# Kernel optimization log

Hardware: AMD Instinct MI355X
Metric: run time of the kernel (lower is better)

Reference implementation:

```python
import jax, jax.numpy as jnp
import numpy as np

T, B, H = 256, 64, 1024

def setup_inputs() -> dict:
    key = jax.random.key(0)
    k0, k1, k2, k3 = jax.random.split(key, 4)
    x = jax.random.normal(k0, (T, B, H), dtype=jnp.float32)
    # episode resets are sparse events
    resets = jax.random.bernoulli(k1, 0.01, (T, B))
    h0 = jnp.zeros((B, H), dtype=jnp.float32)  # flax GRUCell.initialize_carry -> zeros
    s = np.float32(1.0 / np.sqrt(H))
    Wi = jax.random.normal(k2, (H, 3 * H), dtype=jnp.float32) * s  # packed [ir|iz|in]
    Wh = jax.random.normal(k3, (H, 3 * H), dtype=jnp.float32) * s  # packed [hr|hz|hn]
    bi = jnp.zeros((3 * H,), dtype=jnp.float32)
    bn = jnp.zeros((H,), dtype=jnp.float32)  # only the 'n' hidden dense has a bias in flax
    return dict(x=x, resets=resets, h0=h0, Wi=Wi, bi=bi, Wh=Wh, bn=bn)

def reference(x, resets, h0, Wi, bi, Wh, bn):
    """Scanned GRU with reset masking, matching flax nn.scan(GRUCell)."""
    def step(h, inp):
        x_t, r_t = inp  # [B,H], [B]
        h = jnp.where(r_t[:, None], jnp.zeros_like(h), h)  # reset carry to initial (zeros)
        gi = x_t @ Wi + bi          # [B,3H]
        gh = h @ Wh                 # [B,3H]
        ir, iz, inn = jnp.split(gi, 3, axis=-1)
        hr, hz, hn = jnp.split(gh, 3, axis=-1)
        r = jax.nn.sigmoid(ir + hr)
        z = jax.nn.sigmoid(iz + hz)
        n = jnp.tanh(inn + r * (hn + bn))
        h_new = (1.0 - z) * n + z * h
        return h_new, h_new  # GRUCell returns (new_state, y=new_state)
    h_final, ys = jax.lax.scan(step, h0, (x, resets))
    return h_final, ys
```

## Files before the change

### kernel.cpp

```cpp
#include <hip/hip_runtime.h>
#include <hip/hip_bf16.h>
#include <cstdint>


#define TT 256
#define BB 64
#define HH 1024
#define H3 3072

typedef __attribute__((ext_vector_type(8))) short s16x8;
typedef __attribute__((ext_vector_type(4))) float f32x4;
typedef __attribute__((ext_vector_type(4))) unsigned int u32x4;
typedef unsigned long long ull;

__device__ __forceinline__ float fast_sigmoid(float x) {
  float e = __expf(-fabsf(x));
  float s = 1.0f / (1.0f + e);
  return x >= 0.0f ? s : 1.0f - s;
}
__device__ __forceinline__ float fast_tanh(float x) {
  float e = __expf(-2.0f * fabsf(x));
  float t = (1.0f - e) / (1.0f + e);
  return x >= 0.0f ? t : -t;
}
__device__ __forceinline__ f32x4 mfma16(s16x8 a, s16x8 b, f32x4 c) {
  return __builtin_amdgcn_mfma_f32_16x16x32_bf16(a, b, c, 0, 0, 0);
}

#define LD8(p) __hip_atomic_load((p), __ATOMIC_RELAXED, __HIP_MEMORY_SCOPE_AGENT)


__global__ void k_cvt_x(const float* __restrict__ x, __hip_bfloat16* __restrict__ xb, int n) {
  int i = (blockIdx.x * blockDim.x + threadIdx.x) * 4;
  if (i + 3 < n) {
    float4 v = *reinterpret_cast<const float4*>(x + i);
    xb[i + 0] = __float2bfloat16(v.x);
    xb[i + 1] = __float2bfloat16(v.y);
    xb[i + 2] = __float2bfloat16(v.z);
    xb[i + 3] = __float2bfloat16(v.w);
  }
}

__global__ void k_transpose_w(const float* __restrict__ W, __hip_bfloat16* __restrict__ WT) {
  __shared__ float tile[32][33];
  int c0 = blockIdx.x * 32, r0 = blockIdx.y * 32;
  int tx = threadIdx.x & 31, ty = threadIdx.x >> 5;
#pragma unroll
  for (int i = 0; i < 32; i += 8)
    tile[ty + i][tx] = W[(size_t)(r0 + ty + i) * H3 + c0 + tx];
  __syncthreads();
#pragma unroll
  for (int i = 0; i < 32; i += 8)
    WT[(size_t)(c0 + ty + i) * HH + r0 + tx] = __float2bfloat16(tile[tx][ty + i]);
}


template <bool GIF32>
__global__ __launch_bounds__(256, 2) void k_gemm_gi(
    const __hip_bfloat16* __restrict__ A,
    const __hip_bfloat16* __restrict__ Bt,
    const float* __restrict__ bi,
    void* __restrict__ gi)
{
  __shared__ __align__(16) __hip_bfloat16 As[128 * 32];
  __shared__ __align__(16) __hip_bfloat16 Bs[128 * 32];
  const int bid = blockIdx.x;
  const int mt = bid / 24, nt = bid % 24;
  const int m0 = mt * 128, n0 = nt * 128;
  const int tid = threadIdx.x, lane = tid & 63, w = tid >> 6;
  const int wm = w & 1, wn = w >> 1;

  f32x4 acc[4][4];
#pragma unroll
  for (int ai = 0; ai < 4; ++ai)
#pragma unroll
    for (int bj = 0; bj < 4; ++bj) acc[ai][bj] = (f32x4){0.f, 0.f, 0.f, 0.f};

  for (int k0 = 0; k0 < HH; k0 += 32) {
#pragma unroll
    for (int i = 0; i < 2; ++i) {
      const int c = w + i * 4;
      const int idx = c * 64 + lane;
      const int row = idx >> 2, slot = idx & 3;
      __builtin_amdgcn_global_load_lds(
          (const __attribute__((address_space(1))) void*)(A + (size_t)(m0 + row) * HH + k0 + slot * 8),
          (__attribute__((address_space(3))) void*)(As + c * 512), 16, 0, 0);
      __builtin_amdgcn_global_load_lds(
          (const __attribute__((address_space(1))) void*)(Bt + (size_t)(n0 + row) * HH + k0 + slot * 8),
          (__attribute__((address_space(3))) void*)(Bs + c * 512), 16, 0, 0);
    }
    __syncthreads();
    s16x8 af[4], bf[4];
#pragma unroll
    for (int ai = 0; ai < 4; ++ai) {
      int r = wm * 64 + ai * 16 + (lane & 15);
      af[ai] = *reinterpret_cast<const s16x8*>(As + r * 32 + (lane >> 4) * 8);
    }
#pragma unroll
    for (int bj = 0; bj < 4; ++bj) {
      int r = wn * 64 + bj * 16 + (lane & 15);
      bf[bj] = *reinterpret_cast<const s16x8*>(Bs + r * 32 + (lane >> 4) * 8);
    }
#pragma unroll
    for (int ai = 0; ai < 4; ++ai)
#pragma unroll
      for (int bj = 0; bj < 4; ++bj) acc[ai][bj] = mfma16(af[ai], bf[bj], acc[ai][bj]);
    __syncthreads();
  }

#pragma unroll
  for (int ai = 0; ai < 4; ++ai) {
#pragma unroll
    for (int reg = 0; reg < 4; ++reg) {
      const size_t row = (size_t)m0 + wm * 64 + ai * 16 + (lane >> 4) * 4 + reg;
#pragma unroll
      for (int bj = 0; bj < 4; ++bj) {
        const int col = n0 + wn * 64 + bj * 16 + (lane & 15);
        float v = acc[ai][bj][reg] + bi[col];
        if (GIF32)
          reinterpret_cast<float*>(gi)[row * H3 + col] = v;
        else
          reinterpret_cast<__hip_bfloat16*>(gi)[row * H3 + col] = __float2bfloat16(v);
      }
    }
  }
}


template <bool GIF32>
__global__ __launch_bounds__(256, 1) void k_gru(
    const void* __restrict__ gi_,
    const int* __restrict__ resets,
    const float* __restrict__ h0,
    const float* __restrict__ bn,
    const __hip_bfloat16* __restrict__ WhT,
    __hip_bfloat16* hseq,
    float* __restrict__ out)
{
  __shared__ __align__(16) __hip_bfloat16 Bsh[48 * 1024];
  __shared__ __align__(16) f32x4 part[2][4][3][64];
  __shared__ __align__(8) __hip_bfloat16 hsh[16][16];
  const int tid = threadIdx.x;
  const int wave = tid >> 6, lane = tid & 63;
  const int wg = blockIdx.x;
  const int g = (wg & 7) >> 1;
  const int s = ((wg >> 3) << 1) | (wg & 1);
  const int bg0 = g * 16, j0 = s * 16;

  for (int cch = tid; cch < 48 * 128; cch += 256) {
    const int row = cch >> 7, slot = cch & 127;
    const int gate = row >> 4, jj = row & 15;
    u32x4 v = *reinterpret_cast<const u32x4*>(WhT + (size_t)(gate * HH + j0 + jj) * HH + slot * 8);
    const int byte = row * 2048 + ((slot * 16) ^ ((row & 7) << 4));
    *reinterpret_cast<u32x4*>(reinterpret_cast<char*>(Bsh) + byte) = v;
  }

  const int jl = lane & 15;
  const int bh = (lane >> 4) * 4;
  const int prow = lane >> 2, pq = (lane & 3) * 4;
  const int al = lane & 15;
  const int koff = (lane >> 4) * 8;
  const int j = j0 + jl;

  const char* bbase = reinterpret_cast<const char*>(Bsh);
  const int xsw = (jl & 7) << 4;
  const int rb0 = jl * 2048, rb1 = (16 + jl) * 2048, rb2 = (32 + jl) * 2048;

  float hp[4];
  float girC[4], gizC[4], ginC[4];
  int rstEC[4];
  float bnj = 0.f;

  if (wave == 0) {
    bnj = bn[j];
#pragma unroll
    for (int r = 0; r < 4; ++r) hp[r] = h0[(size_t)(bg0 + bh + r) * HH + j0 + jl];
#pragma unroll
    for (int r = 0; r < 4; ++r) hsh[bh + r][jl] = __float2bfloat16(hp[r]);
    ull pv = *reinterpret_cast<const ull*>(&hsh[prow][pq]);
    __hip_atomic_store(reinterpret_cast<ull*>(hseq + (size_t)g * 16384 + prow * HH + j0 + pq),
                       pv, __ATOMIC_RELAXED, __HIP_MEMORY_SCOPE_AGENT);
#pragma unroll
    for (int r = 0; r < 4; ++r) {
      const int b = bg0 + bh + r;
      rstEC[r] = resets[b];
      if (GIF32) {
        const float* grow = reinterpret_cast<const float*>(gi_) + (size_t)b * H3;
        girC[r] = grow[j]; gizC[r] = grow[HH + j]; ginC[r] = grow[2 * HH + j];
      } else {
        const __hip_bfloat16* grow = reinterpret_cast<const __hip_bfloat16*>(gi_) + (size_t)b * H3;
        girC[r] = __bfloat162float(grow[j]);
        gizC[r] = __bfloat162float(grow[HH + j]);
        ginC[r] = __bfloat162float(grow[2 * HH + j]);
      }
    }
  }
  __syncthreads();

  for (int t = 0; t < TT; ++t) {
    const int rstA = resets[t * BB + bg0 + al];
    const __hip_bfloat16* rd = hseq + (size_t)t * 65536 + g * 16384;
    const ull* ch = reinterpret_cast<const ull*>(rd + al * HH + koff) + wave * 64;

    {
      int gq = 0;
      ull can;
      do {
        can = LD8(ch + 57);
      } while (__any((int)(can == ~0ull)) && ++gq < (1 << 22));
    }
    ull w[16];
#pragma unroll
    for (int i = 0; i < 8; ++i) {
      w[2 * i + 0] = LD8(ch + i * 8 + 0);
      w[2 * i + 1] = LD8(ch + i * 8 + 1);
    }
    {
      int gq = 0;
      for (;;) {
        unsigned bad = 0;
#pragma unroll
        for (int i = 0; i < 16; ++i) bad |= (unsigned)(w[i] == ~0ull);
        if (!__any((int)bad) || ++gq >= (1 << 20)) break;
#pragma unroll
        for (int i = 0; i < 8; ++i) {
          w[2 * i + 0] = LD8(ch + i * 8 + 0);
          w[2 * i + 1] = LD8(ch + i * 8 + 1);
        }
      }
    }

    const ull amask = rstA ? 0ull : ~0ull;
    f32x4 aR = {0.f, 0.f, 0.f, 0.f}, aZ = {0.f, 0.f, 0.f, 0.f}, aN = {0.f, 0.f, 0.f, 0.f};
#pragma unroll
    for (int i = 0; i < 8; ++i) {
      const int kk = wave * 8 + i;
      union { ull q[2]; s16x8 v; } u;
      u.q[0] = w[2 * i + 0] & amask;
      u.q[1] = w[2 * i + 1] & amask;
      const int kb = kk * 64 + (lane >> 4) * 16;
      s16x8 b0 = *reinterpret_cast<const s16x8*>(bbase + rb0 + (kb ^ xsw));
      s16x8 b1 = *reinterpret_cast<const s16x8*>(bbase + rb1 + (kb ^ xsw));
      s16x8 b2 = *reinterpret_cast<const s16x8*>(bbase + rb2 + (kb ^ xsw));
      aR = mfma16(u.v, b0, aR);
      aZ = mfma16(u.v, b1, aZ);
      aN = mfma16(u.v, b2, aN);
    }

    const int p = t & 1;
    part[p][wave][0][lane] = aR;
    part[p][wave][1][lane] = aZ;
    part[p][wave][2][lane] = aN;
    __syncthreads();

    if (wave == 0) {
      f32x4 sR = part[p][0][0][lane], sZ = part[p][0][1][lane], sN = part[p][0][2][lane];
#pragma unroll
      for (int ww = 1; ww < 4; ++ww) {
        sR += part[p][ww][0][lane];
        sZ += part[p][ww][1][lane];
        sN += part[p][ww][2][lane];
      }
      float hnew[4];
#pragma unroll
      for (int r = 0; r < 4; ++r) {
        const float hprev = rstEC[r] ? 0.f : hp[r];
        const float rg = fast_sigmoid(girC[r] + sR[r]);
        const float zg = fast_sigmoid(gizC[r] + sZ[r]);
        const float ng = fast_tanh(ginC[r] + rg * (sN[r] + bnj));
        hnew[r] = (1.0f - zg) * ng + zg * hprev;
        hp[r] = hnew[r];
      }
#pragma unroll
      for (int r = 0; r < 4; ++r) hsh[bh + r][jl] = __float2bfloat16(hnew[r]);
      ull pv = *reinterpret_cast<const ull*>(&hsh[prow][pq]);
      __hip_atomic_store(
          reinterpret_cast<ull*>(hseq + (size_t)(t + 1) * 65536 + g * 16384 + prow * HH + j0 + pq),
          pv, __ATOMIC_RELAXED, __HIP_MEMORY_SCOPE_AGENT);

      float* ys = out + 65536 + (size_t)t * 65536;
#pragma unroll
      for (int r = 0; r < 4; ++r)
        __builtin_nontemporal_store(hnew[r], &ys[(size_t)(bg0 + bh + r) * HH + j]);

      const int tn = (t + 1 < TT) ? t + 1 : t;
#pragma unroll
      for (int r = 0; r < 4; ++r) {
        const int b = bg0 + bh + r;
        rstEC[r] = resets[tn * BB + b];
        if (GIF32) {
          const float* grow = reinterpret_cast<const float*>(gi_) + (size_t)(tn * BB + b) * H3;
          girC[r] = grow[j]; gizC[r] = grow[HH + j]; ginC[r] = grow[2 * HH + j];
        } else {
          const __hip_bfloat16* grow =
              reinterpret_cast<const __hip_bfloat16*>(gi_) + (size_t)(tn * BB + b) * H3;
          girC[r] = __bfloat162float(grow[j]);
          gizC[r] = __bfloat162float(grow[HH + j]);
          ginC[r] = __bfloat162float(grow[2 * HH + j]);
        }
      }
    }
  }

  if (wave == 0) {
#pragma unroll
    for (int r = 0; r < 4; ++r)
      out[(size_t)(bg0 + bh + r) * HH + j0 + jl] = hp[r];
  }
}


extern "C" void kernel_launch(void* const* d_in, const int* in_sizes, int n_in,
                              void* d_out, int out_size, void* d_ws, size_t ws_size,
                              hipStream_t stream) {
  const float* x      = (const float*)d_in[0];
  const int* resets   = (const int*)d_in[1];
  const float* h0     = (const float*)d_in[2];
  const float* Wi     = (const float*)d_in[3];
  const float* bi     = (const float*)d_in[4];
  const float* Wh     = (const float*)d_in[5];
  const float* bn     = (const float*)d_in[6];
  (void)in_sizes; (void)n_in; (void)out_size;

  char* ws = (char*)d_ws;
  __hip_bfloat16* xb   = (__hip_bfloat16*)(ws);
  __hip_bfloat16* hseq = (__hip_bfloat16*)(ws);
  __hip_bfloat16* WiT  = (__hip_bfloat16*)(ws + 33685504);
  __hip_bfloat16* WhT  = (__hip_bfloat16*)(ws + 39976960);
  void* gi             = (void*)(ws + 46268416);

  const bool gif32 = ws_size >= 46268416ull + (size_t)16384 * 3072 * 4;

  k_cvt_x<<<16384, 256, 0, stream>>>(x, xb, TT * BB * HH);
  k_transpose_w<<<dim3(96, 32), 256, 0, stream>>>(Wi, WiT);
  k_transpose_w<<<dim3(96, 32), 256, 0, stream>>>(Wh, WhT);
  if (gif32) {
    k_gemm_gi<true><<<3072, 256, 0, stream>>>(xb, WiT, bi, gi);
    hipMemsetAsync(hseq, 0xFF, 33685504, stream);
    k_gru<true><<<256, 256, 0, stream>>>(gi, resets, h0, bn, WhT, hseq, (float*)d_out);
  } else {
    k_gemm_gi<false><<<3072, 256, 0, stream>>>(xb, WiT, bi, gi);
    hipMemsetAsync(hseq, 0xFF, 33685504, stream);
    k_gru<false><<<256, 256, 0, stream>>>(gi, resets, h0, bn, WhT, hseq, (float*)d_out);
  }
}
```

Baseline: 1.413 ms.

## Keep Wh slice in registers, retile GRU blocks, use cache-bypassing sentinel polling

The persistent GRU kernel now gives each block 8 batch rows and 32 hidden columns instead of 16x16. Each wave holds its share of the recurrent weight slice in registers, so the LDS weight buffer and its per-step shared-memory reads go away. Cross-block hidden-state exchange now uses inline-asm loads with cache-scope bits (sc0, escalating to sc0 sc1) and stores written twice, once with sc0 sc1, to make polling and publishing cheaper. A custom sentinel-fill kernel replaces hipMemsetAsync. In exchange, register pressure rises sharply with 48 s16x8 fragments per lane, half the MFMA rows are masked padding, and the code depends on precise hardware cache semantics.

```diff
diff --git a/kernel.cpp b/kernel.cpp
--- a/kernel.cpp
+++ b/kernel.cpp
@@ -27,7 +27,60 @@
   return __builtin_amdgcn_mfma_f32_16x16x32_bf16(a, b, c, 0, 0, 0);
 }
 
-#define LD8(p) __hip_atomic_load((p), __ATOMIC_RELAXED, __HIP_MEMORY_SCOPE_AGENT)
+
+__device__ __forceinline__ u32x4 ld16c(const char* p, bool e) {
+  u32x4 r;
+  if (!e)
+    asm volatile("global_load_dwordx4 %0, %1, off sc0\n\t"
+                 "s_waitcnt vmcnt(0)"
+                 : "=&v"(r) : "v"(p) : "memory");
+  else
+    asm volatile("global_load_dwordx4 %0, %1, off sc0 sc1\n\t"
+                 "s_waitcnt vmcnt(0)"
+                 : "=&v"(r) : "v"(p) : "memory");
+  return r;
+}
+
+__device__ __forceinline__ void ld8_sc0(u32x4 (&W)[8], const char* b) {
+  asm volatile(
+      "global_load_dwordx4 %0, %8, off sc0\n\t"
+      "global_load_dwordx4 %1, %8, off offset:64 sc0\n\t"
+      "global_load_dwordx4 %2, %8, off offset:128 sc0\n\t"
+      "global_load_dwordx4 %3, %8, off offset:192 sc0\n\t"
+      "global_load_dwordx4 %4, %8, off offset:256 sc0\n\t"
+      "global_load_dwordx4 %5, %8, off offset:320 sc0\n\t"
+      "global_load_dwordx4 %6, %8, off offset:384 sc0\n\t"
+      "global_load_dwordx4 %7, %8, off offset:448 sc0\n\t"
+      "s_waitcnt vmcnt(0)"
+      : "=&v"(W[0]), "=&v"(W[1]), "=&v"(W[2]), "=&v"(W[3]),
+        "=&v"(W[4]), "=&v"(W[5]), "=&v"(W[6]), "=&v"(W[7])
+      : "v"(b) : "memory");
+}
+__device__ __forceinline__ void ld8_sc1(u32x4 (&W)[8], const char* b) {
+  asm volatile(
+      "global_load_dwordx4 %0, %8, off sc0 sc1\n\t"
+      "global_load_dwordx4 %1, %8, off offset:64 sc0 sc1\n\t"
+      "global_load_dwordx4 %2, %8, off offset:128 sc0 sc1\n\t"
+      "global_load_dwordx4 %3, %8, off offset:192 sc0 sc1\n\t"
+      "global_load_dwordx4 %4, %8, off offset:256 sc0 sc1\n\t"
+      "global_load_dwordx4 %5, %8, off offset:320 sc0 sc1\n\t"
+      "global_load_dwordx4 %6, %8, off offset:384 sc0 sc1\n\t"
+      "global_load_dwordx4 %7, %8, off offset:448 sc0 sc1\n\t"
+      "s_waitcnt vmcnt(0)"
+      : "=&v"(W[0]), "=&v"(W[1]), "=&v"(W[2]), "=&v"(W[3]),
+        "=&v"(W[4]), "=&v"(W[5]), "=&v"(W[6]), "=&v"(W[7])
+      : "v"(b) : "memory");
+}
+
+__device__ __forceinline__ void st8_pub(char* p, ull v) {
+  asm volatile("global_store_dwordx2 %0, %1, off\n\t"
+               "global_store_dwordx2 %0, %1, off sc0 sc1"
+               :: "v"(p), "v"(v) : "memory");
+}
+
+__device__ __forceinline__ unsigned sentq(const u32x4& v) {
+  return (unsigned)(((v[0] & v[1]) == ~0u) | ((v[2] & v[3]) == ~0u));
+}
 
 
 __global__ void k_cvt_x(const float* __restrict__ x, __hip_bfloat16* __restrict__ xb, int n) {
@@ -52,6 +105,12 @@
 #pragma unroll
   for (int i = 0; i < 32; i += 8)
     WT[(size_t)(c0 + ty + i) * HH + r0 + tx] = __float2bfloat16(tile[tx][ty + i]);
+}
+
+__global__ void k_fill_sentinel(ull* __restrict__ p, int nwords) {
+  int idx = blockIdx.x * blockDim.x + threadIdx.x;
+  for (int i = idx; i < nwords; i += gridDim.x * blockDim.x)
+    __hip_atomic_store(p + i, ~0ull, __ATOMIC_RELAXED, __HIP_MEMORY_SCOPE_AGENT);
 }
 
 
@@ -137,175 +196,162 @@
     __hip_bfloat16* hseq,
     float* __restrict__ out)
 {
-  __shared__ __align__(16) __hip_bfloat16 Bsh[48 * 1024];
-  __shared__ __align__(16) f32x4 part[2][4][3][64];
-  __shared__ __align__(8) __hip_bfloat16 hsh[16][16];
+  __shared__ __align__(16) f32x4 part[2][4][6][32];
+  __shared__ __align__(8) __hip_bfloat16 hshW[4][8][8];
+
   const int tid = threadIdx.x;
   const int wave = tid >> 6, lane = tid & 63;
   const int wg = blockIdx.x;
-  const int g = (wg & 7) >> 1;
-  const int s = ((wg >> 3) << 1) | (wg & 1);
-  const int bg0 = g * 16, j0 = s * 16;
-
-  for (int cch = tid; cch < 48 * 128; cch += 256) {
-    const int row = cch >> 7, slot = cch & 127;
-    const int gate = row >> 4, jj = row & 15;
-    u32x4 v = *reinterpret_cast<const u32x4*>(WhT + (size_t)(gate * HH + j0 + jj) * HH + slot * 8);
-    const int byte = row * 2048 + ((slot * 16) ^ ((row & 7) << 4));
-    *reinterpret_cast<u32x4*>(reinterpret_cast<char*>(Bsh) + byte) = v;
-  }
-
-  const int jl = lane & 15;
-  const int bh = (lane >> 4) * 4;
-  const int prow = lane >> 2, pq = (lane & 3) * 4;
-  const int al = lane & 15;
-  const int koff = (lane >> 4) * 8;
-  const int j = j0 + jl;
-
-  const char* bbase = reinterpret_cast<const char*>(Bsh);
-  const int xsw = (jl & 7) << 4;
-  const int rb0 = jl * 2048, rb1 = (16 + jl) * 2048, rb2 = (32 + jl) * 2048;
-
-  float hp[4];
-  float girC[4], gizC[4], ginC[4];
-  int rstEC[4];
+  const int g = wg & 7;
+  const int s = wg >> 3;
+  const int bg0 = g * 8, j0 = s * 32;
+  const int lq = lane >> 4, lc = lane & 15;
+
+  s16x8 bf[6][8];
+#pragma unroll
+  for (int gate = 0; gate < 3; ++gate)
+#pragma unroll
+    for (int nt = 0; nt < 2; ++nt)
+#pragma unroll
+      for (int kk = 0; kk < 8; ++kk)
+        bf[gate * 2 + nt][kk] = *reinterpret_cast<const s16x8*>(
+            WhT + (size_t)(gate * HH + j0 + nt * 16 + lc) * HH + wave * 256 + kk * 32 + lq * 8);
+
+  const int colg = j0 + 8 * wave + (lane & 7);
+  const int brow0 = bg0 + ((lane >> 3) & 1) * 4;
+  float hp[4], giR[4], giZ[4], giN[4];
+  int rstE[4];
   float bnj = 0.f;
-
-  if (wave == 0) {
-    bnj = bn[j];
-#pragma unroll
-    for (int r = 0; r < 4; ++r) hp[r] = h0[(size_t)(bg0 + bh + r) * HH + j0 + jl];
-#pragma unroll
-    for (int r = 0; r < 4; ++r) hsh[bh + r][jl] = __float2bfloat16(hp[r]);
-    ull pv = *reinterpret_cast<const ull*>(&hsh[prow][pq]);
-    __hip_atomic_store(reinterpret_cast<ull*>(hseq + (size_t)g * 16384 + prow * HH + j0 + pq),
-                       pv, __ATOMIC_RELAXED, __HIP_MEMORY_SCOPE_AGENT);
-#pragma unroll
-    for (int r = 0; r < 4; ++r) {
-      const int b = bg0 + bh + r;
-      rstEC[r] = resets[b];
+  char* const hseqB = reinterpret_cast<char*>(hseq);
+
+  if (lane < 16) {
+    bnj = bn[colg];
+#pragma unroll
+    for (int i = 0; i < 4; ++i) {
+      const int b = brow0 + i;
+      hp[i] = h0[(size_t)b * HH + colg];
+      rstE[i] = resets[b];
       if (GIF32) {
         const float* grow = reinterpret_cast<const float*>(gi_) + (size_t)b * H3;
-        girC[r] = grow[j]; gizC[r] = grow[HH + j]; ginC[r] = grow[2 * HH + j];
+        giR[i] = grow[colg]; giZ[i] = grow[HH + colg]; giN[i] = grow[2 * HH + colg];
       } else {
-        const __hip_bfloat16* grow = reinterpret_cast<const __hip_bfloat16*>(gi_) + (size_t)b * H3;
-        girC[r] = __bfloat162float(grow[j]);
-        gizC[r] = __bfloat162float(grow[HH + j]);
-        ginC[r] = __bfloat162float(grow[2 * HH + j]);
-      }
-    }
-  }
-  __syncthreads();
+        const __hip_bfloat16* grow =
+            reinterpret_cast<const __hip_bfloat16*>(gi_) + (size_t)b * H3;
+        giR[i] = __bfloat162float(grow[colg]);
+        giZ[i] = __bfloat162float(grow[HH + colg]);
+        giN[i] = __bfloat162float(grow[2 * HH + colg]);
+      }
+      hshW[wave][(b - bg0)][lane & 7] = __float2bfloat16(hp[i]);
+    }
+    ull pv = *reinterpret_cast<const ull*>(&hshW[wave][lane >> 1][(lane & 1) * 4]);
+    st8_pub(hseqB + ((size_t)(bg0 + (lane >> 1)) * HH + j0 + 8 * wave + (lane & 1) * 4) * 2, pv);
+  }
+
+  const size_t abyte = ((size_t)(bg0 + (lane & 7)) * HH + wave * 256 + lq * 8) * 2;
+  bool esc = false;
 
   for (int t = 0; t < TT; ++t) {
-    const int rstA = resets[t * BB + bg0 + al];
-    const __hip_bfloat16* rd = hseq + (size_t)t * 65536 + g * 16384;
-    const ull* ch = reinterpret_cast<const ull*>(rd + al * HH + koff) + wave * 64;
+    const int p = t & 1;
+    const int rstA = resets[t * BB + bg0 + (lane & 7)];
+    const char* cb = hseqB + (size_t)t * 131072 + abyte;
 
     {
-      int gq = 0;
-      ull can;
-      do {
-        can = LD8(ch + 57);
-      } while (__any((int)(can == ~0ull)) && ++gq < (1 << 22));
-    }
-    ull w[16];
-#pragma unroll
-    for (int i = 0; i < 8; ++i) {
-      w[2 * i + 0] = LD8(ch + i * 8 + 0);
-      w[2 * i + 1] = LD8(ch + i * 8 + 1);
-    }
+      int it = 0;
+      for (;;) {
+        u32x4 c = ld16c(cb + 448, esc);
+        if (!__any((int)sentq(c))) break;
+        if (++it == 1024) esc = true;
+        if (it > (1 << 21)) break;
+      }
+    }
+    u32x4 w[8];
+    if (!esc) ld8_sc0(w, cb); else ld8_sc1(w, cb);
     {
-      int gq = 0;
+      int vt = 0;
       for (;;) {
         unsigned bad = 0;
 #pragma unroll
-        for (int i = 0; i < 16; ++i) bad |= (unsigned)(w[i] == ~0ull);
-        if (!__any((int)bad) || ++gq >= (1 << 20)) break;
-#pragma unroll
-        for (int i = 0; i < 8; ++i) {
-          w[2 * i + 0] = LD8(ch + i * 8 + 0);
-          w[2 * i + 1] = LD8(ch + i * 8 + 1);
-        }
-      }
-    }
-
-    const ull amask = rstA ? 0ull : ~0ull;
-    f32x4 aR = {0.f, 0.f, 0.f, 0.f}, aZ = {0.f, 0.f, 0.f, 0.f}, aN = {0.f, 0.f, 0.f, 0.f};
-#pragma unroll
-    for (int i = 0; i < 8; ++i) {
-      const int kk = wave * 8 + i;
-      union { ull q[2]; s16x8 v; } u;
-      u.q[0] = w[2 * i + 0] & amask;
-      u.q[1] = w[2 * i + 1] & amask;
-      const int kb = kk * 64 + (lane >> 4) * 16;
-      s16x8 b0 = *reinterpret_cast<const s16x8*>(bbase + rb0 + (kb ^ xsw));
-      s16x8 b1 = *reinterpret_cast<const s16x8*>(bbase + rb1 + (kb ^ xsw));
-      s16x8 b2 = *reinterpret_cast<const s16x8*>(bbase + rb2 + (kb ^ xsw));
-      aR = mfma16(u.v, b0, aR);
-      aZ = mfma16(u.v, b1, aZ);
-      aN = mfma16(u.v, b2, aN);
-    }
-
-    const int p = t & 1;
-    part[p][wave][0][lane] = aR;
-    part[p][wave][1][lane] = aZ;
-    part[p][wave][2][lane] = aN;
+        for (int i = 0; i < 8; ++i) bad |= sentq(w[i]);
+        if (!__any((int)bad)) break;
+        if (++vt == 256) esc = true;
+        if (vt > (1 << 19)) break;
+        if (!esc) ld8_sc0(w, cb); else ld8_sc1(w, cb);
+      }
+    }
+
+    const unsigned vm = (lc < 8 && !rstA) ? ~0u : 0u;
+    f32x4 acc[6];
+#pragma unroll
+    for (int tl = 0; tl < 6; ++tl) acc[tl] = (f32x4){0.f, 0.f, 0.f, 0.f};
+#pragma unroll
+    for (int kk = 0; kk < 8; ++kk) {
+      u32x4 m = w[kk];
+      m[0] &= vm; m[1] &= vm; m[2] &= vm; m[3] &= vm;
+      s16x8 a = __builtin_bit_cast(s16x8, m);
+#pragma unroll
+      for (int tl = 0; tl < 6; ++tl) acc[tl] = mfma16(a, bf[tl][kk], acc[tl]);
+    }
+
+    if (lane < 32) {
+#pragma unroll
+      for (int tl = 0; tl < 6; ++tl) part[p][wave][tl][lane] = acc[tl];
+    }
     __syncthreads();
 
-    if (wave == 0) {
-      f32x4 sR = part[p][0][0][lane], sZ = part[p][0][1][lane], sN = part[p][0][2][lane];
+    if (lane < 16) {
+      const int ntE = wave >> 1;
+      const int pi = ((lane >> 3) << 4) | ((wave & 1) << 3) | (lane & 7);
+      f32x4 sR = part[p][0][ntE][pi];
+      f32x4 sZ = part[p][0][2 + ntE][pi];
+      f32x4 sN = part[p][0][4 + ntE][pi];
 #pragma unroll
       for (int ww = 1; ww < 4; ++ww) {
-        sR += part[p][ww][0][lane];
-        sZ += part[p][ww][1][lane];
-        sN += part[p][ww][2][lane];
+        sR += part[p][ww][ntE][pi];
+        sZ += part[p][ww][2 + ntE][pi];
+        sN += part[p][ww][4 + ntE][pi];
       }
       float hnew[4];
 #pragma unroll
-      for (int r = 0; r < 4; ++r) {
-        const float hprev = rstEC[r] ? 0.f : hp[r];
-        const float rg = fast_sigmoid(girC[r] + sR[r]);
-        const float zg = fast_sigmoid(gizC[r] + sZ[r]);
-        const float ng = fast_tanh(ginC[r] + rg * (sN[r] + bnj));
-        hnew[r] = (1.0f - zg) * ng + zg * hprev;
-        hp[r] = hnew[r];
-      }
-#pragma unroll
-      for (int r = 0; r < 4; ++r) hsh[bh + r][jl] = __float2bfloat16(hnew[r]);
-      ull pv = *reinterpret_cast<const ull*>(&hsh[prow][pq]);
-      __hip_atomic_store(
-          reinterpret_cast<ull*>(hseq + (size_t)(t + 1) * 65536 + g * 16384 + prow * HH + j0 + pq),
-          pv, __ATOMIC_RELAXED, __HIP_MEMORY_SCOPE_AGENT);
-
+      for (int i = 0; i < 4; ++i) {
+        const float hprev = rstE[i] ? 0.f : hp[i];
+        const float rg = fast_sigmoid(giR[i] + sR[i]);
+        const float zg = fast_sigmoid(giZ[i] + sZ[i]);
+        const float ng = fast_tanh(giN[i] + rg * (sN[i] + bnj));
+        hnew[i] = (1.0f - zg) * ng + zg * hprev;
+        hp[i] = hnew[i];
+        hshW[wave][brow0 - bg0 + i][lane & 7] = __float2bfloat16(hnew[i]);
+      }
+      ull pv = *reinterpret_cast<const ull*>(&hshW[wave][lane >> 1][(lane & 1) * 4]);
+      st8_pub(hseqB + (size_t)(t + 1) * 131072 +
+                  ((size_t)(bg0 + (lane >> 1)) * HH + j0 + 8 * wave + (lane & 1) * 4) * 2,
+              pv);
       float* ys = out + 65536 + (size_t)t * 65536;
 #pragma unroll
-      for (int r = 0; r < 4; ++r)
-        __builtin_nontemporal_store(hnew[r], &ys[(size_t)(bg0 + bh + r) * HH + j]);
-
+      for (int i = 0; i < 4; ++i)
+        __builtin_nontemporal_store(hnew[i], &ys[(size_t)(brow0 + i) * HH + colg]);
       const int tn = (t + 1 < TT) ? t + 1 : t;
 #pragma unroll
-      for (int r = 0; r < 4; ++r) {
-        const int b = bg0 + bh + r;
-        rstEC[r] = resets[tn * BB + b];
+      for (int i = 0; i < 4; ++i) {
+        const int b = brow0 + i;
+        rstE[i] = resets[tn * BB + b];
         if (GIF32) {
           const float* grow = reinterpret_cast<const float*>(gi_) + (size_t)(tn * BB + b) * H3;
-          girC[r] = grow[j]; gizC[r] = grow[HH + j]; ginC[r] = grow[2 * HH + j];
+          giR[i] = grow[colg]; giZ[i] = grow[HH + colg]; giN[i] = grow[2 * HH + colg];
         } else {
           const __hip_bfloat16* grow =
               reinterpret_cast<const __hip_bfloat16*>(gi_) + (size_t)(tn * BB + b) * H3;
-          girC[r] = __bfloat162float(grow[j]);
-          gizC[r] = __bfloat162float(grow[HH + j]);
-          ginC[r] = __bfloat162float(grow[2 * HH + j]);
+          giR[i] = __bfloat162float(grow[colg]);
+          giZ[i] = __bfloat162float(grow[HH + colg]);
+          giN[i] = __bfloat162float(grow[2 * HH + colg]);
         }
       }
     }
   }
 
-  if (wave == 0) {
-#pragma unroll
-    for (int r = 0; r < 4; ++r)
-      out[(size_t)(bg0 + bh + r) * HH + j0 + jl] = hp[r];
+  if (lane < 16) {
+#pragma unroll
+    for (int i = 0; i < 4; ++i)
+      out[(size_t)(brow0 + i) * HH + colg] = hp[i];
   }
 }
 
@@ -336,11 +382,11 @@
   k_transpose_w<<<dim3(96, 32), 256, 0, stream>>>(Wh, WhT);
   if (gif32) {
     k_gemm_gi<true><<<3072, 256, 0, stream>>>(xb, WiT, bi, gi);
-    hipMemsetAsync(hseq, 0xFF, 33685504, stream);
+    k_fill_sentinel<<<2048, 256, 0, stream>>>((ull*)hseq, 33685504 / 8);
     k_gru<true><<<256, 256, 0, stream>>>(gi, resets, h0, bn, WhT, hseq, (float*)d_out);
   } else {
     k_gemm_gi<false><<<3072, 256, 0, stream>>>(xb, WiT, bi, gi);
-    hipMemsetAsync(hseq, 0xFF, 33685504, stream);
+    k_fill_sentinel<<<2048, 256, 0, stream>>>((ull*)hseq, 33685504 / 8);
     k_gru<false><<<256, 256, 0, stream>>>(gi, resets, h0, bn, WhT, hseq, (float*)d_out);
   }
 }
```

Result: slower. 2.732 ms (+93.4%).

## Replace sentinel-value polling with per-block step counters for cross-block sync

Applied to the files above, without the earlier changes.

Each block now publishes a monotonic step counter after storing its hidden-state slice, and consumers poll the 64 flags of their batch group instead of checking the hidden-state data for a 0xFF sentinel. This removes the 33 MB sentinel memset before the recurrence kernel and the re-read loop over the loaded data. It relies on relaxed stores plus an s_waitcnt for ordering, which risks visibility races without a release/acquire fence. The poll timeout also drops to 1<<14 iterations.

```diff
diff --git a/kernel.cpp b/kernel.cpp
--- a/kernel.cpp
+++ b/kernel.cpp
@@ -135,6 +135,7 @@
     const float* __restrict__ bn,
     const __hip_bfloat16* __restrict__ WhT,
     __hip_bfloat16* hseq,
+    ull* flags,
     float* __restrict__ out)
 {
   __shared__ __align__(16) __hip_bfloat16 Bsh[48 * 1024];
@@ -146,6 +147,7 @@
   const int g = (wg & 7) >> 1;
   const int s = ((wg >> 3) << 1) | (wg & 1);
   const int bg0 = g * 16, j0 = s * 16;
+  ull* const myflag = flags + g * 64 + s;
 
   for (int cch = tid; cch < 48 * 128; cch += 256) {
     const int row = cch >> 7, slot = cch & 127;
@@ -180,6 +182,9 @@
     ull pv = *reinterpret_cast<const ull*>(&hsh[prow][pq]);
     __hip_atomic_store(reinterpret_cast<ull*>(hseq + (size_t)g * 16384 + prow * HH + j0 + pq),
                        pv, __ATOMIC_RELAXED, __HIP_MEMORY_SCOPE_AGENT);
+    asm volatile("s_waitcnt vmcnt(0)" ::: "memory");
+    if (lane == 0)
+      __hip_atomic_store(myflag, 1ull, __ATOMIC_RELAXED, __HIP_MEMORY_SCOPE_AGENT);
 #pragma unroll
     for (int r = 0; r < 4; ++r) {
       const int b = bg0 + bh + r;
@@ -197,6 +202,8 @@
   }
   __syncthreads();
 
+  const ull* const pollflag = flags + g * 64 + wave * 16 + (lane & 15);
+
   for (int t = 0; t < TT; ++t) {
     const int rstA = resets[t * BB + bg0 + al];
     const __hip_bfloat16* rd = hseq + (size_t)t * 65536 + g * 16384;
@@ -204,30 +211,17 @@
 
     {
       int gq = 0;
-      ull can;
+      ull f;
       do {
-        can = LD8(ch + 57);
-      } while (__any((int)(can == ~0ull)) && ++gq < (1 << 22));
-    }
+        f = LD8(pollflag);
+      } while (__any((int)(f < (ull)(t + 1))) && ++gq < (1 << 14));
+    }
+
     ull w[16];
 #pragma unroll
     for (int i = 0; i < 8; ++i) {
       w[2 * i + 0] = LD8(ch + i * 8 + 0);
       w[2 * i + 1] = LD8(ch + i * 8 + 1);
-    }
-    {
-      int gq = 0;
-      for (;;) {
-        unsigned bad = 0;
-#pragma unroll
-        for (int i = 0; i < 16; ++i) bad |= (unsigned)(w[i] == ~0ull);
-        if (!__any((int)bad) || ++gq >= (1 << 20)) break;
-#pragma unroll
-        for (int i = 0; i < 8; ++i) {
-          w[2 * i + 0] = LD8(ch + i * 8 + 0);
-          w[2 * i + 1] = LD8(ch + i * 8 + 1);
-        }
-      }
     }
 
     const ull amask = rstA ? 0ull : ~0ull;
@@ -277,6 +271,9 @@
       __hip_atomic_store(
           reinterpret_cast<ull*>(hseq + (size_t)(t + 1) * 65536 + g * 16384 + prow * HH + j0 + pq),
           pv, __ATOMIC_RELAXED, __HIP_MEMORY_SCOPE_AGENT);
+      asm volatile("s_waitcnt vmcnt(0)" ::: "memory");
+      if (lane == 0)
+        __hip_atomic_store(myflag, (ull)(t + 2), __ATOMIC_RELAXED, __HIP_MEMORY_SCOPE_AGENT);
 
       float* ys = out + 65536 + (size_t)t * 65536;
 #pragma unroll
@@ -327,20 +324,20 @@
   __hip_bfloat16* hseq = (__hip_bfloat16*)(ws);
   __hip_bfloat16* WiT  = (__hip_bfloat16*)(ws + 33685504);
   __hip_bfloat16* WhT  = (__hip_bfloat16*)(ws + 39976960);
-  void* gi             = (void*)(ws + 46268416);
-
-  const bool gif32 = ws_size >= 46268416ull + (size_t)16384 * 3072 * 4;
-
+  ull* flags           = (ull*)(ws + 46268416);
+  void* gi             = (void*)(ws + 46270464);
+
+  const bool gif32 = ws_size >= 46270464ull + (size_t)16384 * 3072 * 4;
+
+  hipMemsetAsync(flags, 0, 2048, stream);
   k_cvt_x<<<16384, 256, 0, stream>>>(x, xb, TT * BB * HH);
   k_transpose_w<<<dim3(96, 32), 256, 0, stream>>>(Wi, WiT);
   k_transpose_w<<<dim3(96, 32), 256, 0, stream>>>(Wh, WhT);
   if (gif32) {
     k_gemm_gi<true><<<3072, 256, 0, stream>>>(xb, WiT, bi, gi);
-    hipMemsetAsync(hseq, 0xFF, 33685504, stream);
-    k_gru<true><<<256, 256, 0, stream>>>(gi, resets, h0, bn, WhT, hseq, (float*)d_out);
+    k_gru<true><<<256, 256, 0, stream>>>(gi, resets, h0, bn, WhT, hseq, flags, (float*)d_out);
   } else {
     k_gemm_gi<false><<<3072, 256, 0, stream>>>(xb, WiT, bi, gi);
-    hipMemsetAsync(hseq, 0xFF, 33685504, stream);
-    k_gru<false><<<256, 256, 0, stream>>>(gi, resets, h0, bn, WhT, hseq, (float*)d_out);
-  }
-}
+    k_gru<false><<<256, 256, 0, stream>>>(gi, resets, h0, bn, WhT, hseq, flags, (float*)d_out);
+  }
+}
```

After: 1.547 ms. 1.09x slower.

## Spread GRU gate epilogue across all four waves and target canary polling

Applied to the files above, without the earlier changes.

Each step's gate nonlinearity, state update, h publish and next-step gi/reset prefetch now run on all 256 threads, one (batch,hidden) element per thread, instead of only wave 0 handling four elements per lane. Each wave publishes its own four rows of the new hidden state. The spin-wait now polls one word per producer block per wave rather than a single canary word, and the retry caps shrink. This shortens the serial per-step critical path after the partial-sum barrier, at the cost of more polling loads and a possible hazard: hsh is written and read within the step without an intervening barrier.

```diff
diff --git a/kernel.cpp b/kernel.cpp
--- a/kernel.cpp
+++ b/kernel.cpp
@@ -28,6 +28,7 @@
 }
 
 #define LD8(p) __hip_atomic_load((p), __ATOMIC_RELAXED, __HIP_MEMORY_SCOPE_AGENT)
+#define ST8(p, v) __hip_atomic_store((p), (v), __ATOMIC_RELAXED, __HIP_MEMORY_SCOPE_AGENT)
 
 
 __global__ void k_cvt_x(const float* __restrict__ x, __hip_bfloat16* __restrict__ xb, int n) {
@@ -155,60 +156,55 @@
     *reinterpret_cast<u32x4*>(reinterpret_cast<char*>(Bsh) + byte) = v;
   }
 
-  const int jl = lane & 15;
-  const int bh = (lane >> 4) * 4;
-  const int prow = lane >> 2, pq = (lane & 3) * 4;
+  const int bl = tid >> 4;
+  const int jl = tid & 15;
+  const int b = bg0 + bl, j = j0 + jl;
+  const float bnj = bn[j];
+  float hp = h0[(size_t)b * HH + j];
+  int rstE;
+  float giR, giZ, giN;
+  {
+    rstE = resets[b];
+    if (GIF32) {
+      const float* grow = reinterpret_cast<const float*>(gi_) + (size_t)b * H3;
+      giR = grow[j]; giZ = grow[HH + j]; giN = grow[2 * HH + j];
+    } else {
+      const __hip_bfloat16* grow = reinterpret_cast<const __hip_bfloat16*>(gi_) + (size_t)b * H3;
+      giR = __bfloat162float(grow[j]);
+      giZ = __bfloat162float(grow[HH + j]);
+      giN = __bfloat162float(grow[2 * HH + j]);
+    }
+  }
+
+  hsh[bl][jl] = __float2bfloat16(hp);
+  __syncthreads();
+  if (lane < 16) {
+    const int prow = wave * 4 + (lane >> 2), pq = (lane & 3) * 4;
+    ull pv = *reinterpret_cast<const ull*>(&hsh[prow][pq]);
+    ST8(reinterpret_cast<ull*>(hseq + (size_t)g * 16384 + prow * HH + j0 + pq), pv);
+  }
+
   const int al = lane & 15;
   const int koff = (lane >> 4) * 8;
-  const int j = j0 + jl;
-
   const char* bbase = reinterpret_cast<const char*>(Bsh);
   const int xsw = (jl & 7) << 4;
   const int rb0 = jl * 2048, rb1 = (16 + jl) * 2048, rb2 = (32 + jl) * 2048;
-
-  float hp[4];
-  float girC[4], gizC[4], ginC[4];
-  int rstEC[4];
-  float bnj = 0.f;
-
-  if (wave == 0) {
-    bnj = bn[j];
-#pragma unroll
-    for (int r = 0; r < 4; ++r) hp[r] = h0[(size_t)(bg0 + bh + r) * HH + j0 + jl];
-#pragma unroll
-    for (int r = 0; r < 4; ++r) hsh[bh + r][jl] = __float2bfloat16(hp[r]);
-    ull pv = *reinterpret_cast<const ull*>(&hsh[prow][pq]);
-    __hip_atomic_store(reinterpret_cast<ull*>(hseq + (size_t)g * 16384 + prow * HH + j0 + pq),
-                       pv, __ATOMIC_RELAXED, __HIP_MEMORY_SCOPE_AGENT);
-#pragma unroll
-    for (int r = 0; r < 4; ++r) {
-      const int b = bg0 + bh + r;
-      rstEC[r] = resets[b];
-      if (GIF32) {
-        const float* grow = reinterpret_cast<const float*>(gi_) + (size_t)b * H3;
-        girC[r] = grow[j]; gizC[r] = grow[HH + j]; ginC[r] = grow[2 * HH + j];
-      } else {
-        const __hip_bfloat16* grow = reinterpret_cast<const __hip_bfloat16*>(gi_) + (size_t)b * H3;
-        girC[r] = __bfloat162float(grow[j]);
-        gizC[r] = __bfloat162float(grow[HH + j]);
-        ginC[r] = __bfloat162float(grow[2 * HH + j]);
-      }
-    }
-  }
-  __syncthreads();
+  const int cprod = lane & 15, crow = (lane >> 4) * 4 + 1;
 
   for (int t = 0; t < TT; ++t) {
     const int rstA = resets[t * BB + bg0 + al];
     const __hip_bfloat16* rd = hseq + (size_t)t * 65536 + g * 16384;
+
+    {
+      const ull* cp = reinterpret_cast<const ull*>(rd + crow * HH + wave * 256 + cprod * 16 + 8);
+      int gq = 0;
+      ull c;
+      do {
+        c = LD8(cp);
+      } while (__any((int)(c == ~0ull)) && ++gq < (1 << 20));
+    }
+
     const ull* ch = reinterpret_cast<const ull*>(rd + al * HH + koff) + wave * 64;
-
-    {
-      int gq = 0;
-      ull can;
-      do {
-        can = LD8(ch + 57);
-      } while (__any((int)(can == ~0ull)) && ++gq < (1 << 22));
-    }
     ull w[16];
 #pragma unroll
     for (int i = 0; i < 8; ++i) {
@@ -221,7 +217,7 @@
         unsigned bad = 0;
 #pragma unroll
         for (int i = 0; i < 16; ++i) bad |= (unsigned)(w[i] == ~0ull);
-        if (!__any((int)bad) || ++gq >= (1 << 20)) break;
+        if (!__any((int)bad) || ++gq >= (1 << 18)) break;
 #pragma unroll
         for (int i = 0; i < 8; ++i) {
           w[2 * i + 0] = LD8(ch + i * 8 + 0);
@@ -253,60 +249,46 @@
     part[p][wave][2][lane] = aN;
     __syncthreads();
 
-    if (wave == 0) {
-      f32x4 sR = part[p][0][0][lane], sZ = part[p][0][1][lane], sN = part[p][0][2][lane];
-#pragma unroll
-      for (int ww = 1; ww < 4; ++ww) {
-        sR += part[p][ww][0][lane];
-        sZ += part[p][ww][1][lane];
-        sN += part[p][ww][2][lane];
-      }
-      float hnew[4];
-#pragma unroll
-      for (int r = 0; r < 4; ++r) {
-        const float hprev = rstEC[r] ? 0.f : hp[r];
-        const float rg = fast_sigmoid(girC[r] + sR[r]);
-        const float zg = fast_sigmoid(gizC[r] + sZ[r]);
-        const float ng = fast_tanh(ginC[r] + rg * (sN[r] + bnj));
-        hnew[r] = (1.0f - zg) * ng + zg * hprev;
-        hp[r] = hnew[r];
-      }
-#pragma unroll
-      for (int r = 0; r < 4; ++r) hsh[bh + r][jl] = __float2bfloat16(hnew[r]);
+    const int li = ((bl >> 2) << 4) | jl, el = bl & 3;
+    float sR = part[p][0][0][li][el], sZ = part[p][0][1][li][el], sN = part[p][0][2][li][el];
+#pragma unroll
+    for (int ww = 1; ww < 4; ++ww) {
+      sR += part[p][ww][0][li][el];
+      sZ += part[p][ww][1][li][el];
+      sN += part[p][ww][2][li][el];
+    }
+    const float hprev = rstE ? 0.f : hp;
+    const float rg = fast_sigmoid(giR + sR);
+    const float zg = fast_sigmoid(giZ + sZ);
+    const float ng = fast_tanh(giN + rg * (sN + bnj));
+    const float hnew = (1.0f - zg) * ng + zg * hprev;
+    hp = hnew;
+
+    hsh[bl][jl] = __float2bfloat16(hnew);
+    if (lane < 16) {
+      const int prow = wave * 4 + (lane >> 2), pq = (lane & 3) * 4;
       ull pv = *reinterpret_cast<const ull*>(&hsh[prow][pq]);
-      __hip_atomic_store(
-          reinterpret_cast<ull*>(hseq + (size_t)(t + 1) * 65536 + g * 16384 + prow * HH + j0 + pq),
-          pv, __ATOMIC_RELAXED, __HIP_MEMORY_SCOPE_AGENT);
-
-      float* ys = out + 65536 + (size_t)t * 65536;
-#pragma unroll
-      for (int r = 0; r < 4; ++r)
-        __builtin_nontemporal_store(hnew[r], &ys[(size_t)(bg0 + bh + r) * HH + j]);
-
-      const int tn = (t + 1 < TT) ? t + 1 : t;
-#pragma unroll
-      for (int r = 0; r < 4; ++r) {
-        const int b = bg0 + bh + r;
-        rstEC[r] = resets[tn * BB + b];
-        if (GIF32) {
-          const float* grow = reinterpret_cast<const float*>(gi_) + (size_t)(tn * BB + b) * H3;
-          girC[r] = grow[j]; gizC[r] = grow[HH + j]; ginC[r] = grow[2 * HH + j];
-        } else {
-          const __hip_bfloat16* grow =
-              reinterpret_cast<const __hip_bfloat16*>(gi_) + (size_t)(tn * BB + b) * H3;
-          girC[r] = __bfloat162float(grow[j]);
-          gizC[r] = __bfloat162float(grow[HH + j]);
-          ginC[r] = __bfloat162float(grow[2 * HH + j]);
-        }
-      }
-    }
-  }
-
-  if (wave == 0) {
-#pragma unroll
-    for (int r = 0; r < 4; ++r)
-      out[(size_t)(bg0 + bh + r) * HH + j0 + jl] = hp[r];
-  }
+      ST8(reinterpret_cast<ull*>(hseq + (size_t)(t + 1) * 65536 + g * 16384 + prow * HH + j0 + pq),
+          pv);
+    }
+
+    __builtin_nontemporal_store(hnew, out + 65536 + (size_t)t * 65536 + (size_t)b * HH + j);
+
+    const int tn = (t + 1 < TT) ? t + 1 : t;
+    rstE = resets[tn * BB + b];
+    if (GIF32) {
+      const float* grow = reinterpret_cast<const float*>(gi_) + (size_t)(tn * BB + b) * H3;
+      giR = grow[j]; giZ = grow[HH + j]; giN = grow[2 * HH + j];
+    } else {
+      const __hip_bfloat16* grow =
+          reinterpret_cast<const __hip_bfloat16*>(gi_) + (size_t)(tn * BB + b) * H3;
+      giR = __bfloat162float(grow[j]);
+      giZ = __bfloat162float(grow[HH + j]);
+      giN = __bfloat162float(grow[2 * HH + j]);
+    }
+  }
+
+  out[(size_t)b * HH + j] = hp;
 }
 
 
```

Measured after the change: 1.283 ms, median of 2. 9.2% less time.
